# Optimization experiments

Measured on AMD Instinct MI355X. Metric: run time of the kernel, lower is better.

The kernel has to match this reference:

```python
import jax, jax.numpy as jnp
import numpy as np

DIM = 512
HEADS = 8
HEAD_DIM = DIM // HEADS
SCALE = HEAD_DIM ** -0.5
EPS = 1e-5


def setup_inputs() -> dict:
    key = jax.random.key(0)
    ks = jax.random.split(key, 6)
    B, N, C = 4, 2048, DIM
    x = jax.random.normal(ks[0], (B, N, C), dtype=jnp.float32)
    w_qkv = jax.random.normal(ks[1], (C, 3 * C), dtype=jnp.float32) * (C ** -0.5)
    w_proj = jax.random.normal(ks[2], (C, C), dtype=jnp.float32) * (C ** -0.5)
    b_proj = jax.random.normal(ks[3], (C,), dtype=jnp.float32) * 0.02
    gamma = jnp.ones((C,), dtype=jnp.float32)
    beta = jnp.zeros((C,), dtype=jnp.float32)
    return {"x": x, "w_qkv": w_qkv, "w_proj": w_proj, "b_proj": b_proj,
            "gamma": gamma, "beta": beta}


def reference(x, w_qkv, w_proj, b_proj, gamma, beta):
    B, N, C = x.shape
    # LayerNorm over channel dim
    mu = jnp.mean(x, axis=-1, keepdims=True)
    var = jnp.mean(jnp.square(x - mu), axis=-1, keepdims=True)
    xn = (x - mu) * jax.lax.rsqrt(var + EPS) * gamma + beta
    # QKV projection (fp32, no bias)
    qkv = xn @ w_qkv  # [B, N, 3C]
    qkv = qkv.reshape(B, N, 3, HEADS, HEAD_DIM)
    q = jnp.transpose(qkv[:, :, 0], (0, 2, 1, 3))  # [B, H, N, D]
    k = jnp.transpose(qkv[:, :, 1], (0, 2, 1, 3))
    v = jnp.transpose(qkv[:, :, 2], (0, 2, 1, 3))
    attn = jnp.einsum('bhnd,bhmd->bhnm', q, k) * SCALE
    attn = jax.nn.softmax(attn, axis=-1)
    out = jnp.einsum('bhnm,bhmd->bhnd', attn, v)  # [B, H, N, D]
    out = jnp.transpose(out, (0, 2, 1, 3)).reshape(B, N, C)
    out = out @ w_proj + b_proj
    return x + out
```

## Files before the change

### kernel.cpp

```cpp
#include <hip/hip_runtime.h>
#include <hip/hip_bf16.h>
#include <math.h>

typedef _Float16 f16;
typedef _Float16 half8 __attribute__((ext_vector_type(8)));
typedef _Float16 half4 __attribute__((ext_vector_type(4)));
typedef _Float16 half2v __attribute__((ext_vector_type(2)));
typedef float f32x4 __attribute__((ext_vector_type(4)));
typedef unsigned int uint;
typedef unsigned int u32x4 __attribute__((ext_vector_type(4)));

#define DIMC 512
#define HEADS 8
#define HD 64
#define BB 4
#define NN 2048
#define MM (BB*NN)
#define NQKV (3*DIMC)
#define SCALE 0.125f
#define LOG2E 1.44269504f
#define EPSLN 1e-5f
#define NCHUNK 2

__device__ __forceinline__ void g2l16(const void* g, void* l) {
    __builtin_amdgcn_global_load_lds(
        (const __attribute__((address_space(1))) unsigned int*)g,
        (__attribute__((address_space(3))) unsigned int*)l, 16, 0, 0);
}

__device__ __forceinline__ void ln_rows(const float* __restrict__ x,
                                        const float* __restrict__ gamma,
                                        const float* __restrict__ beta,
                                        f16* __restrict__ xn, int blk) {
    int w = threadIdx.x >> 6;
    int lane = threadIdx.x & 63;
    int row = blk * 4 + w;
    const float* xr = x + (size_t)row * DIMC;
    float4 v0 = ((const float4*)xr)[lane * 2];
    float4 v1 = ((const float4*)xr)[lane * 2 + 1];
    float s = v0.x + v0.y + v0.z + v0.w + v1.x + v1.y + v1.z + v1.w;
#pragma unroll
    for (int off = 1; off < 64; off <<= 1) s += __shfl_xor(s, off);
    float mu = s * (1.0f / DIMC);
    float d0 = v0.x - mu, d1 = v0.y - mu, d2 = v0.z - mu, d3 = v0.w - mu;
    float d4 = v1.x - mu, d5 = v1.y - mu, d6 = v1.z - mu, d7 = v1.w - mu;
    float s2 = d0*d0 + d1*d1 + d2*d2 + d3*d3 + d4*d4 + d5*d5 + d6*d6 + d7*d7;
#pragma unroll
    for (int off = 1; off < 64; off <<= 1) s2 += __shfl_xor(s2, off);
    float rstd = rsqrtf(s2 * (1.0f / DIMC) + EPSLN);
    float4 g0 = ((const float4*)gamma)[lane * 2];
    float4 g1 = ((const float4*)gamma)[lane * 2 + 1];
    float4 b0 = ((const float4*)beta)[lane * 2];
    float4 b1 = ((const float4*)beta)[lane * 2 + 1];
    half8 o;
    o[0] = (f16)(d0 * rstd * g0.x + b0.x);
    o[1] = (f16)(d1 * rstd * g0.y + b0.y);
    o[2] = (f16)(d2 * rstd * g0.z + b0.z);
    o[3] = (f16)(d3 * rstd * g0.w + b0.w);
    o[4] = (f16)(d4 * rstd * g1.x + b1.x);
    o[5] = (f16)(d5 * rstd * g1.y + b1.y);
    o[6] = (f16)(d6 * rstd * g1.z + b1.z);
    o[7] = (f16)(d7 * rstd * g1.w + b1.w);
    ((half8*)(xn + (size_t)row * DIMC))[lane] = o;
}

__device__ __forceinline__ void transp_tile(const float* __restrict__ src,
                                            f16* __restrict__ dst,
                                            int R, int C, int k0, int n0) {
    __shared__ f16 t[32][72];
    int tid = threadIdx.x;
    int rr = tid >> 6, col = tid & 63;
#pragma unroll
    for (int p = 0; p < 8; p++) {
        int r = p * 4 + rr;
        t[r][col] = (f16)src[(size_t)(k0 + r) * C + n0 + col];
    }
    __syncthreads();
    int nl = tid >> 2, kc = (tid & 3) * 8;
    half8 v;
#pragma unroll
    for (int j = 0; j < 8; j++) v[j] = t[kc + j][nl];
    *(half8*)&dst[(size_t)(n0 + nl) * R + k0 + kc] = v;
}

__global__ __launch_bounds__(256) void prep_kernel(const float* __restrict__ x,
                                                   const float* __restrict__ gamma,
                                                   const float* __restrict__ beta,
                                                   const float* __restrict__ wqkv,
                                                   const float* __restrict__ wproj,
                                                   f16* __restrict__ xn,
                                                   f16* __restrict__ wqkvt,
                                                   f16* __restrict__ wprojt) {
    int bid = blockIdx.x;
    if (bid < 2048) {
        ln_rows(x, gamma, beta, xn, bid);
    } else if (bid < 2048 + 384) {
        int b2 = bid - 2048;
        int bx = b2 % 24, by = b2 / 24;
        transp_tile(wqkv, wqkvt, DIMC, NQKV, by * 32, bx * 64);
    } else {
        int b2 = bid - 2048 - 384;
        int bx = b2 % 8, by = b2 / 8;
        transp_tile(wproj, wprojt, DIMC, DIMC, by * 32, bx * 64);
    }
}

__device__ __forceinline__ void gemm128_loop(const char* Ag, const char* Bg,
                                             f16* As, f16* Bs, f32x4 (&acc)[4][4]) {
    int tid = threadIdx.x;
    int w = tid >> 6, lane = tid & 63, l15 = lane & 15, quad = lane >> 4;
    int wy = w >> 1, wx = w & 1;
    int off0 = w * 1024 + lane * 16;
    for (int kk = 0; kk < 16; ++kk) {
        __syncthreads();
#pragma unroll
        for (int c = 0; c < 2; ++c) {
            int off = c * 4096 + off0;
            int row = off >> 6, col = off & 63;
            g2l16(Ag + (size_t)row * 1024 + kk * 64 + col, (char*)As + c * 4096 + w * 1024);
            g2l16(Bg + (size_t)row * 1024 + kk * 64 + col, (char*)Bs + c * 4096 + w * 1024);
        }
        __syncthreads();
        half8 af[4], bf[4];
#pragma unroll
        for (int i = 0; i < 4; ++i) {
            af[i] = *(const half8*)((const char*)As + ((wy * 64 + i * 16 + l15) << 6) + quad * 16);
            bf[i] = *(const half8*)((const char*)Bs + ((wx * 64 + i * 16 + l15) << 6) + quad * 16);
        }
#pragma unroll
        for (int i = 0; i < 4; ++i)
#pragma unroll
            for (int j = 0; j < 4; ++j)
                acc[i][j] = __builtin_amdgcn_mfma_f32_16x16x32_f16(af[i], bf[j], acc[i][j], 0, 0, 0);
    }
}

__global__ __launch_bounds__(256) void gemm_qkv(const f16* __restrict__ xn,
                                                const f16* __restrict__ wt,
                                                f16* __restrict__ qb,
                                                f16* __restrict__ kbuf,
                                                f16* __restrict__ vtb) {
    __shared__ __align__(16) f16 As[128 * 32];
    __shared__ __align__(16) f16 Bs[128 * 32];
    int tid = threadIdx.x;
    int w = tid >> 6, lane = tid & 63, l15 = lane & 15, quad = lane >> 4;
    int wy = w >> 1, wx = w & 1;
    int m0 = blockIdx.y * 128, c0 = blockIdx.x * 128;
    f32x4 acc[4][4] = {};
    gemm128_loop((const char*)(xn + (size_t)m0 * DIMC),
                 (const char*)(wt + (size_t)c0 * DIMC), As, Bs, acc);
    int bx = blockIdx.x;
    if (bx < 8) {
        const float QS = SCALE * LOG2E;
        f16* dst = (bx < 4) ? qb : kbuf;
        float mul = (bx < 4) ? QS : 1.0f;
        int cb = (bx < 4) ? c0 : c0 - DIMC;
#pragma unroll
        for (int i = 0; i < 4; ++i)
#pragma unroll
            for (int j = 0; j < 4; ++j)
#pragma unroll
                for (int r = 0; r < 4; ++r) {
                    int m = m0 + wy * 64 + i * 16 + quad * 4 + r;
                    int c = cb + wx * 64 + j * 16 + l15;
                    int b = m >> 11, n = m & 2047;
                    int h = c >> 6, d = c & 63;
                    dst[(((size_t)(b * HEADS + h)) * NN + n) * HD + d] = (f16)(acc[i][j][r] * mul);
                }
    } else {
        __syncthreads();
        f16* T = (f16*)As + w * 512;
        int cb = c0 - 2 * DIMC;
        int dl = lane >> 2, mp = lane & 3;
#pragma unroll
        for (int i = 0; i < 4; ++i)
#pragma unroll
            for (int j = 0; j < 4; ++j) {
                half4 hv;
#pragma unroll
                for (int r = 0; r < 4; ++r) hv[r] = (f16)acc[i][j][r];
                *(half4*)&T[l15 * 20 + quad * 4] = hv;
                half4 rv = *(half4*)&T[dl * 20 + mp * 4];
                int c = cb + wx * 64 + j * 16 + dl;
                int m = m0 + wy * 64 + i * 16 + mp * 4;
                int b = m >> 11, n = m & 2047;
                int h = c >> 6, d = c & 63;
                *(half4*)&vtb[(((size_t)(b * HEADS + h)) * HD + d) * NN + n] = rv;
            }
    }
}

__global__ __launch_bounds__(256, 4) void attn_kernel(const f16* __restrict__ qb,
                                                      const f16* __restrict__ kbuf,
                                                      const f16* __restrict__ vtb,
                                                      f16* __restrict__ po,
                                                      float* __restrict__ pl) {
    __shared__ __align__(16) f16 KV[8192];
    char* Kc = (char*)KV;
    char* Vc = (char*)(KV + 4096);
    int id = blockIdx.x;
    int xcd = id & 7, slot = id >> 3;
    int g = xcd * (4 * NCHUNK) + (slot >> 4);
    int qt4 = slot & 15;
    int bh = g & 31;
    int chunk = g >> 5;
    int n0 = qt4 * 128;
    int tid = threadIdx.x, w = tid >> 6, lane = tid & 63, l15 = lane & 15, quad = lane >> 4;
    const f16* Kbase = kbuf + (size_t)bh * NN * HD;
    const f16* Vbase = vtb + (size_t)bh * HD * NN;
    const f16* Qbase = qb + (size_t)bh * NN * HD;
    half8 qf[2][2];
#pragma unroll
    for (int qt = 0; qt < 2; ++qt) {
        const f16* qr = Qbase + (size_t)(n0 + w * 32 + qt * 16 + l15) * HD + quad * 8;
        qf[qt][0] = *(const half8*)qr;
        qf[qt][1] = *(const half8*)(qr + 32);
    }
    f32x4 ot[2][4] = {};
    f32x4 lacc[2] = {};
    half8 ones8;
#pragma unroll
    for (int j = 0; j < 8; ++j) ones8[j] = (f16)1.0f;
    int srow = tid >> 2, part = (tid & 3) * 16;
    int sb = srow * 128, sx = (srow & 7) << 4;
    int scol = part * 2;
    int rx = (l15 & 7) << 4;
    int kbeg = chunk * (NN / NCHUNK);
    half8 kp0, kp1, vp0, vp1;
    {
        const f16* kg = Kbase + (size_t)(kbeg + srow) * HD + part;
        kp0 = ((const half8*)kg)[0]; kp1 = ((const half8*)kg)[1];
        const f16* vg = Vbase + (size_t)srow * NN + kbeg + part;
        vp0 = ((const half8*)vg)[0]; vp1 = ((const half8*)vg)[1];
    }
    for (int it = 0; it < NN / NCHUNK / 64; ++it) {
        __syncthreads();
        *(half8*)(Kc + sb + (scol ^ sx)) = kp0;
        *(half8*)(Kc + sb + ((scol + 16) ^ sx)) = kp1;
        *(half8*)(Vc + sb + (scol ^ sx)) = vp0;
        *(half8*)(Vc + sb + ((scol + 16) ^ sx)) = vp1;
        __syncthreads();
        if (it < NN / NCHUNK / 64 - 1) {
            int kt0 = kbeg + (it + 1) * 64;
            const f16* kg = Kbase + (size_t)(kt0 + srow) * HD + part;
            kp0 = ((const half8*)kg)[0]; kp1 = ((const half8*)kg)[1];
            const f16* vg = Vbase + (size_t)srow * NN + kt0 + part;
            vp0 = ((const half8*)vg)[0]; vp1 = ((const half8*)vg)[1];
        }
        f32x4 s0[4], s1[4];
        __builtin_amdgcn_s_setprio(1);
#pragma unroll
        for (int kt = 0; kt < 4; ++kt) {
            int rb = (kt * 16 + l15) * 128;
            half8 a0 = *(const half8*)(Kc + rb + ((quad * 16) ^ rx));
            half8 a1 = *(const half8*)(Kc + rb + ((64 + quad * 16) ^ rx));
            f32x4 z0 = {};
            z0 = __builtin_amdgcn_mfma_f32_16x16x32_f16(a0, qf[0][0], z0, 0, 0, 0);
            z0 = __builtin_amdgcn_mfma_f32_16x16x32_f16(a1, qf[0][1], z0, 0, 0, 0);
            s0[kt] = z0;
            f32x4 z1 = {};
            z1 = __builtin_amdgcn_mfma_f32_16x16x32_f16(a0, qf[1][0], z1, 0, 0, 0);
            z1 = __builtin_amdgcn_mfma_f32_16x16x32_f16(a1, qf[1][1], z1, 0, 0, 0);
            s1[kt] = z1;
        }
        __builtin_amdgcn_s_setprio(0);
        uint up[2][4][2];
#pragma unroll
        for (int kt = 0; kt < 4; ++kt) {
            up[0][kt][0] = __builtin_bit_cast(uint, __builtin_amdgcn_cvt_pkrtz(
                __builtin_amdgcn_exp2f(s0[kt][0]), __builtin_amdgcn_exp2f(s0[kt][1])));
            up[0][kt][1] = __builtin_bit_cast(uint, __builtin_amdgcn_cvt_pkrtz(
                __builtin_amdgcn_exp2f(s0[kt][2]), __builtin_amdgcn_exp2f(s0[kt][3])));
            up[1][kt][0] = __builtin_bit_cast(uint, __builtin_amdgcn_cvt_pkrtz(
                __builtin_amdgcn_exp2f(s1[kt][0]), __builtin_amdgcn_exp2f(s1[kt][1])));
            up[1][kt][1] = __builtin_bit_cast(uint, __builtin_amdgcn_cvt_pkrtz(
                __builtin_amdgcn_exp2f(s1[kt][2]), __builtin_amdgcn_exp2f(s1[kt][3])));
        }
        __builtin_amdgcn_s_setprio(1);
#pragma unroll
        for (int kc = 0; kc < 2; ++kc) {
            int cb = (kc * 64 + quad * 16) ^ rx;
            half8 av[4];
#pragma unroll
            for (int dt = 0; dt < 4; ++dt)
                av[dt] = *(const half8*)(Vc + (dt * 16 + l15) * 128 + cb);
#pragma unroll
            for (int qt = 0; qt < 2; ++qt) {
                u32x4 pw;
#pragma unroll
                for (int i = 0; i < 2; ++i) {
                    uint x = up[qt][kc * 2][i], y = up[qt][kc * 2 + 1][i];
                    asm volatile("v_permlane32_swap_b32 %0, %1" : "+v"(x), "+v"(y));
                    asm volatile("v_permlane16_swap_b32 %0, %1" : "+v"(x), "+v"(y));
                    pw[i] = x; pw[2 + i] = y;
                }
                half8 pb8 = __builtin_bit_cast(half8, pw);
                lacc[qt] = __builtin_amdgcn_mfma_f32_16x16x32_f16(ones8, pb8, lacc[qt], 0, 0, 0);
#pragma unroll
                for (int dt = 0; dt < 4; ++dt)
                    ot[qt][dt] = __builtin_amdgcn_mfma_f32_16x16x32_f16(av[dt], pb8, ot[qt][dt], 0, 0, 0);
            }
        }
        __builtin_amdgcn_s_setprio(0);
    }
    size_t rowbase = ((size_t)chunk * (BB * HEADS) + bh) * NN;
#pragma unroll
    for (int qt = 0; qt < 2; ++qt) {
        if (quad == 0) pl[rowbase + n0 + w * 32 + qt * 16 + l15] = lacc[qt][0];
    }
    __syncthreads();
    char* Tc = (char*)(KV + w * 2048);
#pragma unroll
    for (int qt = 0; qt < 2; ++qt)
#pragma unroll
        for (int dt = 0; dt < 4; ++dt) {
            half4 hv;
#pragma unroll
            for (int r = 0; r < 4; ++r) hv[r] = (f16)ot[qt][dt][r];
            *(half4*)(Tc + (qt * 16 + l15) * 128 + ((dt * 32 + quad * 8) ^ rx)) = hv;
        }
    __syncthreads();
#pragma unroll
    for (int j = 0; j < 4; ++j) {
        int nl = j * 8 + (lane >> 3);
        int d16 = (lane & 7) * 16;
        half8 v = *(const half8*)(Tc + nl * 128 + (d16 ^ ((nl & 7) << 4)));
        *(half8*)&po[(rowbase + n0 + w * 32 + nl) * HD + (lane & 7) * 8] = v;
    }
}

__global__ __launch_bounds__(256) void attn_combine(const f16* __restrict__ po,
                                                    const float* __restrict__ pl,
                                                    f16* __restrict__ ao) {
    int gid = blockIdx.x * 256 + threadIdx.x;
    int row = gid >> 3, d0 = (gid & 7) * 8;
    int bh = row >> 11, n = row & 2047;
    const int CS = BB * HEADS * NN;
    float l = 0.f;
#pragma unroll
    for (int c = 0; c < NCHUNK; ++c) l += pl[row + c * CS];
    float inv = 1.0f / l;
    float acc[8] = {};
#pragma unroll
    for (int c = 0; c < NCHUNK; ++c) {
        half8 oc = *(const half8*)&po[((size_t)row + c * CS) * HD + d0];
#pragma unroll
        for (int j = 0; j < 8; ++j) acc[j] += (float)oc[j];
    }
    half8 r;
#pragma unroll
    for (int j = 0; j < 8; ++j) r[j] = (f16)(acc[j] * inv);
    int h = bh & 7, b = bh >> 3;
    *(half8*)&ao[((size_t)(b * NN + n)) * DIMC + h * HD + d0] = r;
}

__global__ __launch_bounds__(256) void gemm_proj(const f16* __restrict__ aob,
                                                 const f16* __restrict__ wt,
                                                 const float* __restrict__ x,
                                                 const float* __restrict__ bias,
                                                 float* __restrict__ out) {
    __shared__ __align__(16) f16 As[128 * 32];
    __shared__ __align__(16) f16 Bs[64 * 32];
    int tid = threadIdx.x;
    int w = tid >> 6, lane = tid & 63, l15 = lane & 15, quad = lane >> 4;
    int m0 = blockIdx.y * 128, c0 = blockIdx.x * 64;
    const char* Ag = (const char*)(aob + (size_t)m0 * DIMC);
    const char* Bg = (const char*)(wt + (size_t)c0 * DIMC);
    f32x4 acc[2][4] = {};
    int off0 = w * 1024 + lane * 16;
    for (int kk = 0; kk < 16; ++kk) {
        __syncthreads();
#pragma unroll
        for (int c = 0; c < 2; ++c) {
            int off = c * 4096 + off0;
            int row = off >> 6, col = off & 63;
            g2l16(Ag + (size_t)row * 1024 + kk * 64 + col, (char*)As + c * 4096 + w * 1024);
        }
        {
            int off = tid * 16;
            int row = off >> 6, col = off & 63;
            g2l16(Bg + (size_t)row * 1024 + kk * 64 + col, (char*)Bs + w * 1024);
        }
        __syncthreads();
        half8 af[2], bf[4];
#pragma unroll
        for (int i = 0; i < 2; ++i)
            af[i] = *(const half8*)((const char*)As + ((w * 32 + i * 16 + l15) << 6) + quad * 16);
#pragma unroll
        for (int j = 0; j < 4; ++j)
            bf[j] = *(const half8*)((const char*)Bs + ((j * 16 + l15) << 6) + quad * 16);
#pragma unroll
        for (int i = 0; i < 2; ++i)
#pragma unroll
            for (int j = 0; j < 4; ++j)
                acc[i][j] = __builtin_amdgcn_mfma_f32_16x16x32_f16(af[i], bf[j], acc[i][j], 0, 0, 0);
    }
#pragma unroll
    for (int i = 0; i < 2; ++i)
#pragma unroll
        for (int j = 0; j < 4; ++j)
#pragma unroll
            for (int r = 0; r < 4; ++r) {
                int m = m0 + w * 32 + i * 16 + quad * 4 + r;
                int c = c0 + j * 16 + l15;
                out[(size_t)m * DIMC + c] = x[(size_t)m * DIMC + c] + bias[c] + acc[i][j][r];
            }
}

extern "C" void kernel_launch(void* const* d_in, const int* in_sizes, int n_in,
                              void* d_out, int out_size, void* d_ws, size_t ws_size,
                              hipStream_t stream) {
    (void)in_sizes; (void)n_in; (void)out_size; (void)ws_size;
    const float* x     = (const float*)d_in[0];
    const float* wqkv  = (const float*)d_in[1];
    const float* wproj = (const float*)d_in[2];
    const float* bproj = (const float*)d_in[3];
    const float* gamma = (const float*)d_in[4];
    const float* beta  = (const float*)d_in[5];
    float* out = (float*)d_out;

    char* ws = (char*)d_ws;
    f16* xn     = (f16*)ws;                 ws += (size_t)MM * DIMC * 2;
    f16* wqkvt  = (f16*)ws;                 ws += (size_t)NQKV * DIMC * 2;
    f16* wprojt = (f16*)ws;                 ws += (size_t)DIMC * DIMC * 2;
    f16* qbuf   = (f16*)ws;                 ws += (size_t)MM * DIMC * 2;
    f16* kbuf   = (f16*)ws;                 ws += (size_t)MM * DIMC * 2;
    f16* vtbuf  = (f16*)ws;                 ws += (size_t)MM * DIMC * 2;
    f16* aobuf  = (f16*)ws;                 ws += (size_t)MM * DIMC * 2;
    f16* po     = (f16*)ws;                 ws += (size_t)NCHUNK * BB * HEADS * NN * HD * 2;
    float* pl   = (float*)ws;               ws += (size_t)NCHUNK * BB * HEADS * NN * sizeof(float);

    prep_kernel<<<2048 + 384 + 128, 256, 0, stream>>>(x, gamma, beta, wqkv, wproj,
                                                      xn, wqkvt, wprojt);
    gemm_qkv<<<dim3(NQKV / 128, MM / 128), 256, 0, stream>>>(xn, wqkvt, qbuf, kbuf, vtbuf);
    attn_kernel<<<NN / 128 * BB * HEADS * NCHUNK, 256, 0, stream>>>(qbuf, kbuf, vtbuf, po, pl);
    attn_combine<<<(BB * HEADS * NN * HD / 8) / 256, 256, 0, stream>>>(po, pl, aobuf);
    gemm_proj<<<dim3(DIMC / 64, MM / 128), 256, 0, stream>>>(aobuf, wprojt, x, bproj, out);
}
```

Measured before the change: 162.9 us.

## Drop split-KV attention and fuse normalization into attention epilogue

Removes the two-chunk split over the key dimension, so each attention block processes the full key range. The final 1/l normalization moves into the attention kernel, which writes directly into the projection input layout, and the separate combine kernel and its partial buffers are eliminated. This saves a kernel launch and the partial-output memory traffic. In exchange, the attention grid is halved and each block runs twice as many iterations, which reduces parallelism and latency hiding across CUs.

```diff
diff --git a/kernel.cpp b/kernel.cpp
--- a/kernel.cpp
+++ b/kernel.cpp
@@ -5,7 +5,6 @@
 typedef _Float16 f16;
 typedef _Float16 half8 __attribute__((ext_vector_type(8)));
 typedef _Float16 half4 __attribute__((ext_vector_type(4)));
-typedef _Float16 half2v __attribute__((ext_vector_type(2)));
 typedef float f32x4 __attribute__((ext_vector_type(4)));
 typedef unsigned int uint;
 typedef unsigned int u32x4 __attribute__((ext_vector_type(4)));
@@ -20,7 +19,6 @@
 #define SCALE 0.125f
 #define LOG2E 1.44269504f
 #define EPSLN 1e-5f
-#define NCHUNK 2
 
 __device__ __forceinline__ void g2l16(const void* g, void* l) {
     __builtin_amdgcn_global_load_lds(
@@ -193,17 +191,14 @@
 __global__ __launch_bounds__(256, 4) void attn_kernel(const f16* __restrict__ qb,
                                                       const f16* __restrict__ kbuf,
                                                       const f16* __restrict__ vtb,
-                                                      f16* __restrict__ po,
-                                                      float* __restrict__ pl) {
+                                                      f16* __restrict__ ao) {
     __shared__ __align__(16) f16 KV[8192];
     char* Kc = (char*)KV;
     char* Vc = (char*)(KV + 4096);
     int id = blockIdx.x;
     int xcd = id & 7, slot = id >> 3;
-    int g = xcd * (4 * NCHUNK) + (slot >> 4);
+    int bh = xcd * 4 + (slot >> 4);
     int qt4 = slot & 15;
-    int bh = g & 31;
-    int chunk = g >> 5;
     int n0 = qt4 * 128;
     int tid = threadIdx.x, w = tid >> 6, lane = tid & 63, l15 = lane & 15, quad = lane >> 4;
     const f16* Kbase = kbuf + (size_t)bh * NN * HD;
@@ -225,23 +220,22 @@
     int sb = srow * 128, sx = (srow & 7) << 4;
     int scol = part * 2;
     int rx = (l15 & 7) << 4;
-    int kbeg = chunk * (NN / NCHUNK);
     half8 kp0, kp1, vp0, vp1;
     {
-        const f16* kg = Kbase + (size_t)(kbeg + srow) * HD + part;
+        const f16* kg = Kbase + (size_t)srow * HD + part;
         kp0 = ((const half8*)kg)[0]; kp1 = ((const half8*)kg)[1];
-        const f16* vg = Vbase + (size_t)srow * NN + kbeg + part;
+        const f16* vg = Vbase + (size_t)srow * NN + part;
         vp0 = ((const half8*)vg)[0]; vp1 = ((const half8*)vg)[1];
     }
-    for (int it = 0; it < NN / NCHUNK / 64; ++it) {
+    for (int it = 0; it < NN / 64; ++it) {
         __syncthreads();
         *(half8*)(Kc + sb + (scol ^ sx)) = kp0;
         *(half8*)(Kc + sb + ((scol + 16) ^ sx)) = kp1;
         *(half8*)(Vc + sb + (scol ^ sx)) = vp0;
         *(half8*)(Vc + sb + ((scol + 16) ^ sx)) = vp1;
         __syncthreads();
-        if (it < NN / NCHUNK / 64 - 1) {
-            int kt0 = kbeg + (it + 1) * 64;
+        if (it < NN / 64 - 1) {
+            int kt0 = (it + 1) * 64;
             const f16* kg = Kbase + (size_t)(kt0 + srow) * HD + part;
             kp0 = ((const half8*)kg)[0]; kp1 = ((const half8*)kg)[1];
             const f16* vg = Vbase + (size_t)srow * NN + kt0 + part;
@@ -303,11 +297,7 @@
         }
         __builtin_amdgcn_s_setprio(0);
     }
-    size_t rowbase = ((size_t)chunk * (BB * HEADS) + bh) * NN;
-#pragma unroll
-    for (int qt = 0; qt < 2; ++qt) {
-        if (quad == 0) pl[rowbase + n0 + w * 32 + qt * 16 + l15] = lacc[qt][0];
-    }
+    float inv[2] = { 1.0f / lacc[0][0], 1.0f / lacc[1][0] };
     __syncthreads();
     char* Tc = (char*)(KV + w * 2048);
 #pragma unroll
@@ -316,42 +306,19 @@
         for (int dt = 0; dt < 4; ++dt) {
             half4 hv;
 #pragma unroll
-            for (int r = 0; r < 4; ++r) hv[r] = (f16)ot[qt][dt][r];
+            for (int r = 0; r < 4; ++r) hv[r] = (f16)(ot[qt][dt][r] * inv[qt]);
             *(half4*)(Tc + (qt * 16 + l15) * 128 + ((dt * 32 + quad * 8) ^ rx)) = hv;
         }
     __syncthreads();
+    int b = bh >> 3, h = bh & 7;
 #pragma unroll
     for (int j = 0; j < 4; ++j) {
         int nl = j * 8 + (lane >> 3);
         int d16 = (lane & 7) * 16;
         half8 v = *(const half8*)(Tc + nl * 128 + (d16 ^ ((nl & 7) << 4)));
-        *(half8*)&po[(rowbase + n0 + w * 32 + nl) * HD + (lane & 7) * 8] = v;
-    }
-}
-
-__global__ __launch_bounds__(256) void attn_combine(const f16* __restrict__ po,
-                                                    const float* __restrict__ pl,
-                                                    f16* __restrict__ ao) {
-    int gid = blockIdx.x * 256 + threadIdx.x;
-    int row = gid >> 3, d0 = (gid & 7) * 8;
-    int bh = row >> 11, n = row & 2047;
-    const int CS = BB * HEADS * NN;
-    float l = 0.f;
-#pragma unroll
-    for (int c = 0; c < NCHUNK; ++c) l += pl[row + c * CS];
-    float inv = 1.0f / l;
-    float acc[8] = {};
-#pragma unroll
-    for (int c = 0; c < NCHUNK; ++c) {
-        half8 oc = *(const half8*)&po[((size_t)row + c * CS) * HD + d0];
-#pragma unroll
-        for (int j = 0; j < 8; ++j) acc[j] += (float)oc[j];
-    }
-    half8 r;
-#pragma unroll
-    for (int j = 0; j < 8; ++j) r[j] = (f16)(acc[j] * inv);
-    int h = bh & 7, b = bh >> 3;
-    *(half8*)&ao[((size_t)(b * NN + n)) * DIMC + h * HD + d0] = r;
+        int n = n0 + w * 32 + nl;
+        *(half8*)&ao[((size_t)(b * NN + n)) * DIMC + h * HD + (lane & 7) * 8] = v;
+    }
 }
 
 __global__ __launch_bounds__(256) void gemm_proj(const f16* __restrict__ aob,
@@ -427,13 +394,10 @@
     f16* kbuf   = (f16*)ws;                 ws += (size_t)MM * DIMC * 2;
     f16* vtbuf  = (f16*)ws;                 ws += (size_t)MM * DIMC * 2;
     f16* aobuf  = (f16*)ws;                 ws += (size_t)MM * DIMC * 2;
-    f16* po     = (f16*)ws;                 ws += (size_t)NCHUNK * BB * HEADS * NN * HD * 2;
-    float* pl   = (float*)ws;               ws += (size_t)NCHUNK * BB * HEADS * NN * sizeof(float);
 
     prep_kernel<<<2048 + 384 + 128, 256, 0, stream>>>(x, gamma, beta, wqkv, wproj,
                                                       xn, wqkvt, wprojt);
     gemm_qkv<<<dim3(NQKV / 128, MM / 128), 256, 0, stream>>>(xn, wqkvt, qbuf, kbuf, vtbuf);
-    attn_kernel<<<NN / 128 * BB * HEADS * NCHUNK, 256, 0, stream>>>(qbuf, kbuf, vtbuf, po, pl);
-    attn_combine<<<(BB * HEADS * NN * HD / 8) / 256, 256, 0, stream>>>(po, pl, aobuf);
+    attn_kernel<<<NN / 128 * BB * HEADS, 256, 0, stream>>>(qbuf, kbuf, vtbuf, aobuf);
     gemm_proj<<<dim3(DIMC / 64, MM / 128), 256, 0, stream>>>(aobuf, wprojt, x, bproj, out);
 }
```

Measured after the change: 156.5 us. 1.04x faster.
